# Kernel tuning notes

Hardware: AMD Instinct MI355X
Metric: run time of the kernel (lower is better)

## Reference

```python
import jax, jax.numpy as jnp
import numpy as np

B, S, D = 1, 2048, 4096
H, KVH, DH = 32, 8, 128          # nheads, kv heads, head dim (GQA expansion = 4)
HID = 11008                       # 256 * ceil(4096 * (8/3) / 256)
EPS = 1e-5
ROPE_BASE = 10000.0


def setup_inputs() -> dict:
    key = jax.random.key(0)
    ks = jax.random.split(key, 10)
    std = 0.02
    w = lambda k, shape: jax.random.normal(k, shape, dtype=jnp.float32) * std
    return {
        "x": jax.random.normal(ks[0], (B, S, D), dtype=jnp.float32),
        "position_ids": jnp.broadcast_to(jnp.arange(S, dtype=jnp.int32), (B, S)),
        "ln_w": jnp.ones((D,), dtype=jnp.float32),
        "ffln_w": jnp.ones((D,), dtype=jnp.float32),
        "wq": w(ks[1], (D, H * DH)),
        "wk": w(ks[2], (D, KVH * DH)),
        "wv": w(ks[3], (D, KVH * DH)),
        "wo": w(ks[4], (H * DH, D)),
        "wg": w(ks[5], (D, HID)),
        "w1": w(ks[6], (D, HID)),
        "w2": w(ks[7], (HID, D)),
    }


def rmsnorm(x, w, eps=EPS):
    # LayerNormParameterized(use_mean=False, use_high_precision_pow=True)
    xf = x.astype(jnp.float32)
    var = jnp.mean(xf * xf, axis=-1, keepdims=True)
    return (xf * jax.lax.rsqrt(var + eps)).astype(x.dtype) * w


def rope(x, pos):
    # interleaved (complex-pair) rotary embedding; x: [B,S,h,DH], pos: [B,S]
    dh = x.shape[-1]
    inv_freq = 1.0 / (ROPE_BASE ** (jnp.arange(0, dh, 2, dtype=jnp.float32) / dh))
    ang = pos.astype(jnp.float32)[:, :, None, None] * inv_freq  # [B,S,1,dh/2]
    cos, sin = jnp.cos(ang), jnp.sin(ang)
    x1, x2 = x[..., 0::2], x[..., 1::2]
    return jnp.stack([x1 * cos - x2 * sin, x1 * sin + x2 * cos], axis=-1).reshape(x.shape)


def block(x, position_ids, ln_w, ffln_w, wq, wk, wv, wo, wg, w1, w2):
    # --- attention sublayer ---
    a = rmsnorm(x, ln_w)
    q = (a @ wq).reshape(B, S, H, DH)
    k = (a @ wk).reshape(B, S, KVH, DH)
    v = (a @ wv).reshape(B, S, KVH, DH)
    q = rope(q, position_ids)
    k = rope(k, position_ids)
    # GQA expansion: kv head g serves query heads [g*exp, (g+1)*exp)
    exp = H // KVH
    k_e = jnp.repeat(k, exp, axis=2)  # [B,S,H,DH]
    v_e = jnp.repeat(v, exp, axis=2)
    scores = jnp.einsum("bqhd,bkhd->bhqk", q, k_e) / np.sqrt(DH).astype(np.float32)
    causal = jnp.tril(jnp.ones((S, S), dtype=bool))
    scores = jnp.where(causal, scores, jnp.finfo(scores.dtype).min)
    p = jax.nn.softmax(scores, axis=-1)
    attn = jnp.einsum("bhqk,bkhd->bqhd", p, v_e).reshape(B, S, H * DH)
    x = x + attn @ wo
    # --- SwiGLU FFN sublayer ---
    b = rmsnorm(x, ffln_w)
    ff = (jax.nn.silu(b @ wg) * (b @ w1)) @ w2
    return x + ff


def reference(x, position_ids, ln_w, ffln_w, wq, wk, wv, wo, wg, w1, w2):
    return block(x, position_ids, ln_w, ffln_w, wq, wk, wv, wo, wg, w1, w2)
```

## Files before the change

### kernel.cpp

```cpp
#include <hip/hip_runtime.h>
#include <hip/hip_bf16.h>

typedef __bf16 bf16_t;
typedef __bf16 bf16x4 __attribute__((ext_vector_type(4)));
typedef __bf16 bf16x8 __attribute__((ext_vector_type(8)));
typedef float f32x4 __attribute__((ext_vector_type(4)));

#define S_ 2048
#define D_ 4096
#define H_ 32
#define KVH_ 8
#define DH_ 128
#define HID_ 11008
#define QKV_N 6144
#define GU_N 22016

__device__ __forceinline__ void gl16(const bf16_t* g, bf16_t* l) {
  __builtin_amdgcn_global_load_lds(
      (const __attribute__((address_space(1))) unsigned int*)g,
      (__attribute__((address_space(3))) unsigned int*)l, 16, 0, 0);
}

__global__ __launch_bounds__(256) void rmsnorm_kernel(
    const float* __restrict__ x, const float* __restrict__ w,
    bf16_t* __restrict__ out) {
  int row = blockIdx.x;
  const float* xr = x + (size_t)row * D_;
  float ss = 0.f;
  #pragma unroll
  for (int it = 0; it < 4; ++it) {
    int i = threadIdx.x * 4 + it * 1024;
    float4 v = *(const float4*)(xr + i);
    ss += v.x * v.x + v.y * v.y + v.z * v.z + v.w * v.w;
  }
  #pragma unroll
  for (int off = 32; off; off >>= 1) ss += __shfl_xor(ss, off);
  __shared__ float s4[4];
  if ((threadIdx.x & 63) == 0) s4[threadIdx.x >> 6] = ss;
  __syncthreads();
  float tot = s4[0] + s4[1] + s4[2] + s4[3];
  float rinv = rsqrtf(tot / (float)D_ + 1e-5f);
  bf16_t* orow = out + (size_t)row * D_;
  #pragma unroll
  for (int it = 0; it < 4; ++it) {
    int i = threadIdx.x * 4 + it * 1024;
    float4 v = *(const float4*)(xr + i);
    orow[i + 0] = (bf16_t)(v.x * rinv * w[i + 0]);
    orow[i + 1] = (bf16_t)(v.y * rinv * w[i + 1]);
    orow[i + 2] = (bf16_t)(v.z * rinv * w[i + 2]);
    orow[i + 3] = (bf16_t)(v.w * rinv * w[i + 3]);
  }
}

__global__ __launch_bounds__(256) void combine_rms_kernel(
    const float* __restrict__ x, const float* __restrict__ p0,
    const float* __restrict__ p1, const float* __restrict__ w,
    float* __restrict__ x1, bf16_t* __restrict__ out) {
  int row = blockIdx.x;
  size_t base = (size_t)row * D_;
  float ss = 0.f;
  float4 vals[4];
  #pragma unroll
  for (int it = 0; it < 4; ++it) {
    int i = threadIdx.x * 4 + it * 1024;
    float4 a = *(const float4*)(x + base + i);
    float4 b = *(const float4*)(p0 + base + i);
    float4 c = *(const float4*)(p1 + base + i);
    float4 v;
    v.x = a.x + b.x + c.x; v.y = a.y + b.y + c.y;
    v.z = a.z + b.z + c.z; v.w = a.w + b.w + c.w;
    vals[it] = v;
    *(float4*)(x1 + base + i) = v;
    ss += v.x * v.x + v.y * v.y + v.z * v.z + v.w * v.w;
  }
  #pragma unroll
  for (int off = 32; off; off >>= 1) ss += __shfl_xor(ss, off);
  __shared__ float s4[4];
  if ((threadIdx.x & 63) == 0) s4[threadIdx.x >> 6] = ss;
  __syncthreads();
  float tot = s4[0] + s4[1] + s4[2] + s4[3];
  float rinv = rsqrtf(tot / (float)D_ + 1e-5f);
  #pragma unroll
  for (int it = 0; it < 4; ++it) {
    int i = threadIdx.x * 4 + it * 1024;
    float4 v = vals[it];
    out[base + i + 0] = (bf16_t)(v.x * rinv * w[i + 0]);
    out[base + i + 1] = (bf16_t)(v.y * rinv * w[i + 1]);
    out[base + i + 2] = (bf16_t)(v.z * rinv * w[i + 2]);
    out[base + i + 3] = (bf16_t)(v.w * rinv * w[i + 3]);
  }
}

__global__ __launch_bounds__(256) void combine_out_kernel(
    const float* __restrict__ x1, const float* __restrict__ p0,
    const float* __restrict__ p1, float* __restrict__ outp) {
  size_t i = ((size_t)blockIdx.x * 256 + threadIdx.x) * 4;
  float4 a = *(const float4*)(x1 + i);
  float4 b = *(const float4*)(p0 + i);
  float4 c = *(const float4*)(p1 + i);
  float4 v;
  v.x = a.x + b.x + c.x; v.y = a.y + b.y + c.y;
  v.z = a.z + b.z + c.z; v.w = a.w + b.w + c.w;
  *(float4*)(outp + i) = v;
}

__global__ __launch_bounds__(256) void wtrans_kernel(
    const float* __restrict__ W, bf16_t* __restrict__ WT, int K, int N) {
  __shared__ bf16_t t[32][258];
  int k0 = blockIdx.x * 32, n0 = blockIdx.y * 256;
  #pragma unroll
  for (int i = 0; i < 8; ++i) {
    int flat = i * 1024 + threadIdx.x * 4;
    int kk = flat >> 8, nn = flat & 255;
    float4 wv = *(const float4*)(W + (size_t)(k0 + kk) * N + n0 + nn);
    bf16_t* p = &t[kk][nn];
    p[0] = (bf16_t)wv.x; p[1] = (bf16_t)wv.y;
    p[2] = (bf16_t)wv.z; p[3] = (bf16_t)wv.w;
  }
  __syncthreads();
  int kc8 = (threadIdx.x & 3) * 8;
  #pragma unroll
  for (int i = 0; i < 4; ++i) {
    int nn = i * 64 + (threadIdx.x >> 2);
    bf16x8 vals;
    #pragma unroll
    for (int j = 0; j < 8; ++j) vals[j] = t[kc8 + j][nn];
    *(bf16x8*)(WT + (size_t)(n0 + nn) * K + k0 + kc8) = vals;
  }
}

__global__ __launch_bounds__(256) void rope_table_kernel(
    const int* __restrict__ pos_ids, float* __restrict__ cos_t,
    float* __restrict__ sin_t) {
  int idx = blockIdx.x * 256 + threadIdx.x;
  int s = idx >> 6, i = idx & 63;
  float pos = (float)pos_ids[s];
  float inv_freq = exp2f(-(float)i * (13.287712379549449f / 64.0f));
  float ang = pos * inv_freq;
  cos_t[idx] = cosf(ang);
  sin_t[idx] = sinf(ang);
}

__global__ __launch_bounds__(256) void rope_kernel(
    bf16_t* __restrict__ buf, const float* __restrict__ cos_t,
    const float* __restrict__ sin_t, int nheads, int colbase, int total) {
  int idx = blockIdx.x * 256 + threadIdx.x;
  if (idx >= total) return;
  int i = idx & 63;
  int t2 = idx >> 6;
  int s = t2 / nheads, h = t2 % nheads;
  size_t base = (size_t)s * QKV_N + colbase + h * 128 + 2 * i;
  float x1 = (float)buf[base], x2 = (float)buf[base + 1];
  float c = cos_t[s * 64 + i], sn = sin_t[s * 64 + i];
  buf[base]     = (bf16_t)(x1 * c - x2 * sn);
  buf[base + 1] = (bf16_t)(x1 * sn + x2 * c);
}


#define VMW(N)                                          \
  asm volatile("s_waitcnt vmcnt(" #N ")" ::: "memory"); \
  __builtin_amdgcn_sched_barrier(0)

#define DO_PHASE(BI, KK, MH, DO_LDB, STAGE1, STAGE2, WAITCODE)             \
  {                                                                        \
    _Pragma("unroll") for (int m = 0; m < 4; ++m)                          \
      aF[m] = *(const bf16x8*)&lds[BI][0][wr][KK]                          \
          [((MH) * 64 + m * 16 + fr) * 32 + rc * 8];                       \
    if (DO_LDB) {                                                          \
      _Pragma("unroll") for (int n = 0; n < 4; ++n)                        \
        bF[n] = *(const bf16x8*)&lds[BI][1][wcH][KK]                       \
            [(wcL * 64 + n * 16 + fr) * 32 + rc * 8];                      \
    }                                                                      \
    STAGE1;                                                                \
    STAGE2;                                                                \
    asm volatile("" ::: "memory");                                         \
    __builtin_amdgcn_s_barrier();                                          \
    asm volatile("s_waitcnt lgkmcnt(0)" ::: "memory");                     \
    __builtin_amdgcn_sched_barrier(0);                                     \
    __builtin_amdgcn_s_setprio(1);                                         \
    _Pragma("unroll") for (int m = 0; m < 4; ++m)                          \
      _Pragma("unroll") for (int n = 0; n < 4; ++n)                        \
        acc[(MH) * 4 + m][n] = __builtin_amdgcn_mfma_f32_16x16x32_bf16(    \
            aF[m], bF[n], acc[(MH) * 4 + m][n], 0, 0, 0);                  \
    __builtin_amdgcn_s_setprio(0);                                         \
    __builtin_amdgcn_sched_barrier(0);                                     \
    WAITCODE;                                                              \
    asm volatile("" ::: "memory");                                         \
    __builtin_amdgcn_s_barrier();                                          \
    asm volatile("" ::: "memory");                                         \
  }

#define DO_TILE(BI, T)                                                     \
  {                                                                        \
    const int Tp1 = (T) + 1 < NT, Tp2 = (T) + 2 < NT;                      \
    DO_PHASE(BI, 0, 0, 1,                                                  \
             if (Tp1) stage(BI ^ 1, 0, 0, 1, (T) + 1),                     \
             if (Tp1) stage(BI ^ 1, 1, 0, 1, (T) + 1), );                  \
    DO_PHASE(BI, 0, 1, 0,                                                  \
             if (Tp1) stage(BI ^ 1, 0, 1, 1, (T) + 1),                     \
             if (Tp1) stage(BI ^ 1, 1, 1, 1, (T) + 1),                     \
             if (Tp1) { VMW(8); } else { VMW(0); });                       \
    DO_PHASE(BI, 1, 0, 1,                                                  \
             if (Tp2) stage(BI, 0, 0, 0, (T) + 2),                         \
             if (Tp2) stage(BI, 1, 0, 0, (T) + 2), );                      \
    DO_PHASE(BI, 1, 1, 0,                                                  \
             if (Tp2) stage(BI, 0, 1, 0, (T) + 2),                         \
             if (Tp2) stage(BI, 1, 1, 0, (T) + 2),                         \
             if (Tp2) { VMW(8); } else if (Tp1) { VMW(4); });              \
  }

template <int MODE, int SPLIT>
__global__ __launch_bounds__(512, 2) void gemm256_kernel(
    const bf16_t* __restrict__ A, int lda, const bf16_t* __restrict__ BT,
    int ldb, void* __restrict__ Cout, int ldc, int K) {
  __shared__ __align__(16) bf16_t lds[2][2][2][2][128 * 32];

  const int tid = threadIdx.x;
  const int lane = tid & 63;
  const int wid = tid >> 6;
  const int wr = wid >> 2;
  const int wc = wid & 3;
  const int wcH = wc >> 1, wcL = wc & 1;
  const int g = lane >> 4, fr = lane & 15;
  const int rc = (g + ((fr >> 1) & 3)) & 3;

  const int nwg = gridDim.x;
  const int orig = blockIdx.x;
  int wg = (orig & 7) * (nwg >> 3) + (orig >> 3);
  int kz = 0;
  if constexpr (SPLIT) {
    const int half = nwg >> 1;
    kz = wg >= half;
    wg -= kz * half;
  }
  const int bx = wg & 7;
  const int by = wg >> 3;
  const size_t row0 = (size_t)bx * 256, col0 = (size_t)by * 256;

  const int srow = tid >> 2;
  const int schunk = ((tid & 3) - ((tid >> 3) & 3)) & 3;

  const size_t lda2 = (size_t)lda * 2, ldb2 = (size_t)ldb * 2;
  const size_t kzoff = (size_t)kz * K * 2;
  const char* aB0 =
      (const char*)A + (row0 + srow) * lda2 + schunk * 16 + kzoff;
  const char* aB1 = aB0 + (size_t)128 * lda2;
  const char* bB0 =
      (const char*)BT + (col0 + srow) * ldb2 + schunk * 16 + kzoff;
  const char* bB1 = bB0 + (size_t)128 * ldb2;

  auto stage = [&](int bi, int ab, int h, int kk, int kt) {
    const char* base = ab ? (h ? bB1 : bB0) : (h ? aB1 : aB0);
    gl16((const bf16_t*)(base + (size_t)kt * 128 + kk * 64),
         &lds[bi][ab][h][kk][tid * 8]);
  };

  f32x4 acc[8][4] = {};
  bf16x8 aF[4], bF[4];
  const int NT = K / 64;

  stage(0, 0, 0, 0, 0); stage(0, 1, 0, 0, 0);
  stage(0, 0, 1, 0, 0); stage(0, 1, 1, 0, 0);
  stage(0, 0, 0, 1, 0); stage(0, 1, 0, 1, 0);
  stage(0, 0, 1, 1, 0); stage(0, 1, 1, 1, 0);
  stage(1, 0, 0, 0, 1); stage(1, 1, 0, 0, 1);
  stage(1, 0, 1, 0, 1); stage(1, 1, 1, 0, 1);
  VMW(4);
  asm volatile("" ::: "memory");
  __builtin_amdgcn_s_barrier();
  asm volatile("" ::: "memory");

  for (int T = 0; T < NT; T += 2) {
    DO_TILE(0, T);
    DO_TILE(1, T + 1);
  }

  float* fOut = (float*)Cout + (size_t)kz * 2048 * ldc;
  #pragma unroll
  for (int mf = 0; mf < 8; ++mf)
    #pragma unroll
    for (int n = 0; n < 4; ++n)
      #pragma unroll
      for (int r = 0; r < 4; ++r) {
        size_t row = row0 + wr * 128 + mf * 16 + g * 4 + r;
        size_t col = col0 + wc * 64 + n * 16 + fr;
        float val = acc[mf][n][r];
        if constexpr (MODE == 0) {
          ((bf16_t*)Cout)[row * ldc + col] = (bf16_t)val;
        } else {
          fOut[row * ldc + col] = val;
        }
      }
}

__global__ __launch_bounds__(256) void attn_kernel(
    const bf16_t* __restrict__ qkv, bf16_t* __restrict__ o) {
  int h = blockIdx.y;
  int qb = blockIdx.x;
  int kvh = h >> 2;
  int wid = threadIdx.x >> 6, lane = threadIdx.x & 63;
  int g = lane >> 4, fr = lane & 15;

  __shared__ __align__(16) bf16_t k_lds[64][136];
  __shared__ __align__(16) bf16_t vt_lds[128][72];
  __shared__ __align__(16) bf16_t p_lds[4][16][72];

  int q0w = qb * 64 + wid * 16;
  bf16x8 q_frag[4];
  const bf16_t* qptr = qkv + (size_t)(q0w + fr) * QKV_N + h * 128;
  #pragma unroll
  for (int kc = 0; kc < 4; ++kc)
    q_frag[kc] = *(const bf16x8*)(qptr + kc * 32 + g * 8);

  f32x4 o_frag[8] = {};
  float m_run[4], l_run[4];
  #pragma unroll
  for (int r = 0; r < 4; ++r) { m_run[r] = -1e30f; l_run[r] = 0.f; }

  const float sc = 0.08838834764831845f * 1.4426950408889634f;

  for (int t = 0; t <= qb; ++t) {
    int kv0 = t * 64;
    __syncthreads();
    for (int i = threadIdx.x; i < 1024; i += 256) {
      int row = i >> 4, c8 = (i & 15) * 8;
      size_t base = (size_t)(kv0 + row) * QKV_N + kvh * 128 + c8;
      bf16x8 k8 = *(const bf16x8*)(qkv + base + 4096);
      *(bf16x8*)&k_lds[row][c8] = k8;
      bf16x8 v8 = *(const bf16x8*)(qkv + base + 5120);
      #pragma unroll
      for (int j = 0; j < 8; ++j) vt_lds[c8 + j][row] = v8[j];
    }
    __syncthreads();

    f32x4 sfr[4];
    #pragma unroll
    for (int nf = 0; nf < 4; ++nf) {
      f32x4 acc = {};
      #pragma unroll
      for (int kc = 0; kc < 4; ++kc) {
        bf16x8 kf = *(const bf16x8*)&k_lds[fr + 16 * nf][kc * 32 + g * 8];
        acc = __builtin_amdgcn_mfma_f32_16x16x32_bf16(q_frag[kc], kf, acc, 0, 0, 0);
      }
      sfr[nf] = acc;
    }

    bool diag = (t == qb);
    float mtile[4];
    #pragma unroll
    for (int r = 0; r < 4; ++r) mtile[r] = -1e30f;
    #pragma unroll
    for (int nf = 0; nf < 4; ++nf)
      #pragma unroll
      for (int r = 0; r < 4; ++r) {
        if (diag) {
          int kvg = kv0 + nf * 16 + fr;
          int qg = q0w + 4 * g + r;
          if (kvg > qg) sfr[nf][r] = -1e30f;
        }
        mtile[r] = fmaxf(mtile[r], sfr[nf][r]);
      }
    #pragma unroll
    for (int r = 0; r < 4; ++r) {
      float mv = mtile[r];
      mv = fmaxf(mv, __shfl_xor(mv, 1));
      mv = fmaxf(mv, __shfl_xor(mv, 2));
      mv = fmaxf(mv, __shfl_xor(mv, 4));
      mv = fmaxf(mv, __shfl_xor(mv, 8));
      mtile[r] = mv;
    }
    float alpha[4];
    #pragma unroll
    for (int r = 0; r < 4; ++r) {
      float m_new = fmaxf(m_run[r], mtile[r]);
      alpha[r] = exp2f((m_run[r] - m_new) * sc);
      m_run[r] = m_new;
    }
    float lsum[4] = {0.f, 0.f, 0.f, 0.f};
    #pragma unroll
    for (int nf = 0; nf < 4; ++nf)
      #pragma unroll
      for (int r = 0; r < 4; ++r) {
        float p = exp2f((sfr[nf][r] - m_run[r]) * sc);
        sfr[nf][r] = p;
        lsum[r] += p;
      }
    #pragma unroll
    for (int r = 0; r < 4; ++r) {
      float lv = lsum[r];
      lv += __shfl_xor(lv, 1);
      lv += __shfl_xor(lv, 2);
      lv += __shfl_xor(lv, 4);
      lv += __shfl_xor(lv, 8);
      l_run[r] = l_run[r] * alpha[r] + lv;
    }
    #pragma unroll
    for (int nfo = 0; nfo < 8; ++nfo)
      #pragma unroll
      for (int r = 0; r < 4; ++r) o_frag[nfo][r] *= alpha[r];

    #pragma unroll
    for (int nf = 0; nf < 4; ++nf)
      #pragma unroll
      for (int r = 0; r < 4; ++r)
        p_lds[wid][4 * g + r][nf * 16 + fr] = (bf16_t)sfr[nf][r];
    __syncthreads();

    #pragma unroll
    for (int kc = 0; kc < 2; ++kc) {
      bf16x8 pf = *(const bf16x8*)&p_lds[wid][fr][kc * 32 + g * 8];
      #pragma unroll
      for (int nfo = 0; nfo < 8; ++nfo) {
        bf16x8 vf = *(const bf16x8*)&vt_lds[nfo * 16 + fr][kc * 32 + g * 8];
        o_frag[nfo] = __builtin_amdgcn_mfma_f32_16x16x32_bf16(pf, vf, o_frag[nfo], 0, 0, 0);
      }
    }
  }

  #pragma unroll
  for (int nfo = 0; nfo < 8; ++nfo)
    #pragma unroll
    for (int r = 0; r < 4; ++r) {
      int qg = q0w + 4 * g + r;
      float val = o_frag[nfo][r] / l_run[r];
      o[(size_t)qg * (H_ * DH_) + h * DH_ + nfo * 16 + fr] = (bf16_t)val;
    }
}

__global__ __launch_bounds__(256) void silu_mul_kernel(bf16_t* __restrict__ gu) {
  size_t idx = (size_t)blockIdx.x * 256 + threadIdx.x;
  int r = (int)(idx / (HID_ / 8));
  int c8 = (int)(idx % (HID_ / 8));
  bf16_t* p = gu + (size_t)r * GU_N + c8 * 8;
  bf16x8 g8 = *(const bf16x8*)p;
  bf16x8 u8 = *(const bf16x8*)(p + HID_);
  bf16x8 h8;
  #pragma unroll
  for (int j = 0; j < 8; ++j) {
    float gv = (float)g8[j];
    float uv = (float)u8[j];
    h8[j] = (bf16_t)(gv / (1.f + __expf(-gv)) * uv);
  }
  *(bf16x8*)p = h8;
}

extern "C" void kernel_launch(void* const* d_in, const int* in_sizes, int n_in,
                              void* d_out, int out_size, void* d_ws,
                              size_t ws_size, hipStream_t stream) {
  const float* x = (const float*)d_in[0];
  const int* pos = (const int*)d_in[1];
  const float* ln_w = (const float*)d_in[2];
  const float* ffln_w = (const float*)d_in[3];
  const float* wq = (const float*)d_in[4];
  const float* wk = (const float*)d_in[5];
  const float* wv = (const float*)d_in[6];
  const float* wo = (const float*)d_in[7];
  const float* wg = (const float*)d_in[8];
  const float* w1 = (const float*)d_in[9];
  const float* w2 = (const float*)d_in[10];

  char* ws = (char*)d_ws;
  size_t off = 0;
  auto alloc = [&](size_t bytes) {
    size_t o = off;
    off = (off + bytes + 255) & ~(size_t)255;
    return o;
  };
  bf16_t* Wbuf = (bf16_t*)(ws + alloc((size_t)GU_N * D_ * 2));
  bf16_t* nbuf = (bf16_t*)(ws + alloc((size_t)S_ * D_ * 2));
  bf16_t* qkv  = (bf16_t*)(ws + alloc((size_t)S_ * QKV_N * 2));
  float*  x1   = (float*)(ws + alloc((size_t)S_ * D_ * 4));
  bf16_t* gu   = (bf16_t*)(ws + alloc((size_t)S_ * GU_N * 2));
  float*  cos_t = (float*)(ws + alloc((size_t)S_ * 64 * 4));
  float*  sin_t = (float*)(ws + alloc((size_t)S_ * 64 * 4));
  float* part = (float*)((char*)Wbuf + ((size_t)96 << 20));

  rmsnorm_kernel<<<S_, 256, 0, stream>>>(x, ln_w, nbuf);
  wtrans_kernel<<<dim3(D_ / 32, D_ / 256), 256, 0, stream>>>(wq, Wbuf, D_, D_);
  wtrans_kernel<<<dim3(D_ / 32, 1024 / 256), 256, 0, stream>>>(
      wk, Wbuf + (size_t)4096 * D_, D_, 1024);
  wtrans_kernel<<<dim3(D_ / 32, 1024 / 256), 256, 0, stream>>>(
      wv, Wbuf + (size_t)5120 * D_, D_, 1024);
  rope_table_kernel<<<(S_ * 64) / 256, 256, 0, stream>>>(pos, cos_t, sin_t);
  gemm256_kernel<0, 0><<<dim3((S_ / 256) * (QKV_N / 256)), 512, 0, stream>>>(
      nbuf, D_, Wbuf, D_, qkv, QKV_N, D_);
  rope_kernel<<<(S_ * H_ * 64) / 256, 256, 0, stream>>>(
      qkv, cos_t, sin_t, H_, 0, S_ * H_ * 64);
  rope_kernel<<<(S_ * KVH_ * 64) / 256, 256, 0, stream>>>(
      qkv, cos_t, sin_t, KVH_, 4096, S_ * KVH_ * 64);
  attn_kernel<<<dim3(S_ / 64, H_), 256, 0, stream>>>(qkv, nbuf);
  wtrans_kernel<<<dim3(D_ / 32, D_ / 256), 256, 0, stream>>>(wo, Wbuf, D_, D_);
  gemm256_kernel<2, 1><<<dim3((S_ / 256) * (D_ / 256) * 2), 512, 0, stream>>>(
      nbuf, D_, Wbuf, D_, part, D_, 2048);
  combine_rms_kernel<<<S_, 256, 0, stream>>>(
      x, part, part + (size_t)S_ * D_, ffln_w, x1, nbuf);
  wtrans_kernel<<<dim3(D_ / 32, HID_ / 256), 256, 0, stream>>>(wg, Wbuf, D_, HID_);
  wtrans_kernel<<<dim3(D_ / 32, HID_ / 256), 256, 0, stream>>>(
      w1, Wbuf + (size_t)HID_ * D_, D_, HID_);
  gemm256_kernel<0, 0><<<dim3((S_ / 256) * (GU_N / 256)), 512, 0, stream>>>(
      nbuf, D_, Wbuf, D_, gu, GU_N, D_);
  silu_mul_kernel<<<(S_ * HID_ / 8) / 256, 256, 0, stream>>>(gu);
  wtrans_kernel<<<dim3(HID_ / 32, D_ / 256), 256, 0, stream>>>(w2, Wbuf, HID_, D_);
  gemm256_kernel<2, 1><<<dim3((S_ / 256) * (D_ / 256) * 2), 512, 0, stream>>>(
      gu, GU_N, Wbuf, HID_, part, D_, 5504);
  combine_out_kernel<<<(S_ * D_ / 4) / 256, 256, 0, stream>>>(
      x1, part, part + (size_t)S_ * D_, (float*)d_out);
}
```

Measured before the change: 1.394 ms.

## Double-buffer attention K/V tiles via async global-to-LDS loads with pre-transposed V

Adds a separate kernel that transposes V once into a head-major layout. The attention kernel then prefetches the next K/V tile straight into LDS with global_load_lds into a double buffer, overlapping the copy with the MFMA work on the current tile. It also launches query blocks in reverse order so the longest causal blocks start first, and sets launch bounds for two blocks per CU. The cost is an extra kernel launch, another workspace buffer and more LDS per block.

Result: faster. 1.195 ms (-14.3%).

```diff
diff --git a/kernel.cpp b/kernel.cpp
--- a/kernel.cpp
+++ b/kernel.cpp
@@ -20,6 +20,15 @@
       (const __attribute__((address_space(1))) unsigned int*)g,
       (__attribute__((address_space(3))) unsigned int*)l, 16, 0, 0);
 }
+
+#define VMW(N)                                          \
+  asm volatile("s_waitcnt vmcnt(" #N ")" ::: "memory"); \
+  __builtin_amdgcn_sched_barrier(0)
+
+#define BAR()                          \
+  asm volatile("" ::: "memory");       \
+  __builtin_amdgcn_s_barrier();        \
+  asm volatile("" ::: "memory")
 
 __global__ __launch_bounds__(256) void rmsnorm_kernel(
     const float* __restrict__ x, const float* __restrict__ w,
@@ -126,6 +135,29 @@
     #pragma unroll
     for (int j = 0; j < 8; ++j) vals[j] = t[kc8 + j][nn];
     *(bf16x8*)(WT + (size_t)(n0 + nn) * K + k0 + kc8) = vals;
+  }
+}
+
+__global__ __launch_bounds__(256) void vtrans_kernel(
+    const bf16_t* __restrict__ qkv, bf16_t* __restrict__ vt) {
+  __shared__ bf16_t t[64][72];
+  int s0 = blockIdx.x * 64, d0 = blockIdx.y * 64;
+  #pragma unroll
+  for (int it = 0; it < 2; ++it) {
+    int r = (threadIdx.x >> 3) + it * 32;
+    int c = (threadIdx.x & 7) * 8;
+    *(bf16x8*)&t[r][c] =
+        *(const bf16x8*)(qkv + (size_t)(s0 + r) * QKV_N + 5120 + d0 + c);
+  }
+  __syncthreads();
+  #pragma unroll
+  for (int it = 0; it < 2; ++it) {
+    int c = threadIdx.x & 63;
+    int sb = (threadIdx.x >> 6) * 16 + it * 8;
+    bf16x8 v;
+    #pragma unroll
+    for (int j = 0; j < 8; ++j) v[j] = t[sb + j][c];
+    *(bf16x8*)(vt + (size_t)(d0 + c) * S_ + s0 + sb) = v;
   }
 }
 
@@ -155,11 +187,6 @@
   buf[base]     = (bf16_t)(x1 * c - x2 * sn);
   buf[base + 1] = (bf16_t)(x1 * sn + x2 * c);
 }
-
-
-#define VMW(N)                                          \
-  asm volatile("s_waitcnt vmcnt(" #N ")" ::: "memory"); \
-  __builtin_amdgcn_sched_barrier(0)
 
 #define DO_PHASE(BI, KK, MH, DO_LDB, STAGE1, STAGE2, WAITCODE)             \
   {                                                                        \
@@ -266,9 +293,7 @@
   stage(1, 0, 0, 0, 1); stage(1, 1, 0, 0, 1);
   stage(1, 0, 1, 0, 1); stage(1, 1, 1, 0, 1);
   VMW(4);
-  asm volatile("" ::: "memory");
-  __builtin_amdgcn_s_barrier();
-  asm volatile("" ::: "memory");
+  BAR();
 
   for (int T = 0; T < NT; T += 2) {
     DO_TILE(0, T);
@@ -293,17 +318,38 @@
       }
 }
 
-__global__ __launch_bounds__(256) void attn_kernel(
-    const bf16_t* __restrict__ qkv, bf16_t* __restrict__ o) {
+__global__ __launch_bounds__(256, 2) void attn_kernel(
+    const bf16_t* __restrict__ qkv, const bf16_t* __restrict__ vt,
+    bf16_t* __restrict__ o) {
   int h = blockIdx.y;
-  int qb = blockIdx.x;
+  int qb = (S_ / 64 - 1) - blockIdx.x;
   int kvh = h >> 2;
-  int wid = threadIdx.x >> 6, lane = threadIdx.x & 63;
+  int tid = threadIdx.x;
+  int wid = tid >> 6, lane = tid & 63;
   int g = lane >> 4, fr = lane & 15;
 
-  __shared__ __align__(16) bf16_t k_lds[64][136];
-  __shared__ __align__(16) bf16_t vt_lds[128][72];
+  __shared__ __align__(16) bf16_t kfl[2][8192];
+  __shared__ __align__(16) bf16_t vfl[2][8192];
   __shared__ __align__(16) bf16_t p_lds[4][16][72];
+
+  const int fr_s = (tid >> 2) & 15, g_s = tid & 3;
+  const int kcw = (tid >> 6) & 3;
+  const int kc2w = (tid >> 6) & 1;
+  const int nhi = tid >> 7;
+  const bf16_t* kSrc = qkv + (size_t)fr_s * QKV_N + 4096 + kvh * 128 +
+                       (kcw * 4 + g_s) * 8;
+  const bf16_t* vSrc = vt + ((size_t)kvh * 128 + nhi * 16 + fr_s) * S_ +
+                       (kc2w * 4 + g_s) * 8;
+
+  auto stage = [&](int bi, int t) {
+    size_t kv0 = (size_t)t * 64;
+    #pragma unroll
+    for (int i = 0; i < 4; ++i)
+      gl16(kSrc + (kv0 + i * 16) * QKV_N, &kfl[bi][(i * 256 + tid) * 8]);
+    #pragma unroll
+    for (int i = 0; i < 4; ++i)
+      gl16(vSrc + (size_t)i * 32 * S_ + kv0, &vfl[bi][(i * 256 + tid) * 8]);
+  };
 
   int q0w = qb * 64 + wid * 16;
   bf16x8 q_frag[4];
@@ -311,6 +357,9 @@
   #pragma unroll
   for (int kc = 0; kc < 4; ++kc)
     q_frag[kc] = *(const bf16x8*)(qptr + kc * 32 + g * 8);
+  VMW(0);
+
+  stage(0, 0);
 
   f32x4 o_frag[8] = {};
   float m_run[4], l_run[4];
@@ -320,18 +369,15 @@
   const float sc = 0.08838834764831845f * 1.4426950408889634f;
 
   for (int t = 0; t <= qb; ++t) {
+    int cur = t & 1;
     int kv0 = t * 64;
-    __syncthreads();
-    for (int i = threadIdx.x; i < 1024; i += 256) {
-      int row = i >> 4, c8 = (i & 15) * 8;
-      size_t base = (size_t)(kv0 + row) * QKV_N + kvh * 128 + c8;
-      bf16x8 k8 = *(const bf16x8*)(qkv + base + 4096);
-      *(bf16x8*)&k_lds[row][c8] = k8;
-      bf16x8 v8 = *(const bf16x8*)(qkv + base + 5120);
-      #pragma unroll
-      for (int j = 0; j < 8; ++j) vt_lds[c8 + j][row] = v8[j];
-    }
-    __syncthreads();
+    if (t < qb) {
+      stage(cur ^ 1, t + 1);
+      VMW(8);
+    } else {
+      VMW(0);
+    }
+    BAR();
 
     f32x4 sfr[4];
     #pragma unroll
@@ -339,7 +385,8 @@
       f32x4 acc = {};
       #pragma unroll
       for (int kc = 0; kc < 4; ++kc) {
-        bf16x8 kf = *(const bf16x8*)&k_lds[fr + 16 * nf][kc * 32 + g * 8];
+        bf16x8 kf =
+            *(const bf16x8*)&kfl[cur][(nf * 256 + kc * 64 + fr * 4 + g) * 8];
         acc = __builtin_amdgcn_mfma_f32_16x16x32_bf16(q_frag[kc], kf, acc, 0, 0, 0);
       }
       sfr[nf] = acc;
@@ -404,17 +451,18 @@
       #pragma unroll
       for (int r = 0; r < 4; ++r)
         p_lds[wid][4 * g + r][nf * 16 + fr] = (bf16_t)sfr[nf][r];
-    __syncthreads();
-
-    #pragma unroll
-    for (int kc = 0; kc < 2; ++kc) {
-      bf16x8 pf = *(const bf16x8*)&p_lds[wid][fr][kc * 32 + g * 8];
+
+    #pragma unroll
+    for (int kc2 = 0; kc2 < 2; ++kc2) {
+      bf16x8 pf = *(const bf16x8*)&p_lds[wid][fr][kc2 * 32 + g * 8];
       #pragma unroll
       for (int nfo = 0; nfo < 8; ++nfo) {
-        bf16x8 vf = *(const bf16x8*)&vt_lds[nfo * 16 + fr][kc * 32 + g * 8];
+        bf16x8 vf =
+            *(const bf16x8*)&vfl[cur][(nfo * 128 + kc2 * 64 + fr * 4 + g) * 8];
         o_frag[nfo] = __builtin_amdgcn_mfma_f32_16x16x32_bf16(pf, vf, o_frag[nfo], 0, 0, 0);
       }
     }
+    BAR();
   }
 
   #pragma unroll
@@ -471,6 +519,7 @@
   bf16_t* qkv  = (bf16_t*)(ws + alloc((size_t)S_ * QKV_N * 2));
   float*  x1   = (float*)(ws + alloc((size_t)S_ * D_ * 4));
   bf16_t* gu   = (bf16_t*)(ws + alloc((size_t)S_ * GU_N * 2));
+  bf16_t* vtb  = (bf16_t*)(ws + alloc((size_t)KVH_ * DH_ * S_ * 2));
   float*  cos_t = (float*)(ws + alloc((size_t)S_ * 64 * 4));
   float*  sin_t = (float*)(ws + alloc((size_t)S_ * 64 * 4));
   float* part = (float*)((char*)Wbuf + ((size_t)96 << 20));
@@ -488,7 +537,8 @@
       qkv, cos_t, sin_t, H_, 0, S_ * H_ * 64);
   rope_kernel<<<(S_ * KVH_ * 64) / 256, 256, 0, stream>>>(
       qkv, cos_t, sin_t, KVH_, 4096, S_ * KVH_ * 64);
-  attn_kernel<<<dim3(S_ / 64, H_), 256, 0, stream>>>(qkv, nbuf);
+  vtrans_kernel<<<dim3(S_ / 64, (KVH_ * DH_) / 64), 256, 0, stream>>>(qkv, vtb);
+  attn_kernel<<<dim3(S_ / 64, H_), 256, 0, stream>>>(qkv, vtb, nbuf);
   wtrans_kernel<<<dim3(D_ / 32, D_ / 256), 256, 0, stream>>>(wo, Wbuf, D_, D_);
   gemm256_kernel<2, 1><<<dim3((S_ / 256) * (D_ / 256) * 2), 512, 0, stream>>>(
       nbuf, D_, Wbuf, D_, part, D_, 2048);
```
